# Performance work log

Hardware: AMD Instinct MI355X
Metric: run time of the kernel (lower is better)

The kernel has to match this reference:

```python
import jax, jax.numpy as jnp
import numpy as np
import math

N_HEADS = 8
NUM_LAYERS = 2
OUT_LEN = 96
MIN_FACTOR, MAX_FACTOR = 3, 10
MIN_KERNEL, MAX_KERNEL = 5, 51
LN_EPS = 1e-5


def layer_norm(x, g, b):
    mu = x.mean(-1, keepdims=True)
    var = x.var(-1, keepdims=True)  # biased, like nn.LayerNorm
    return (x - mu) / jnp.sqrt(var + LN_EPS) * g + b


def prob_sparse_attn(x, wq, bq, wk, bk, wv, bv, wo, bo):
    B, L, D = x.shape
    H, dk = N_HEADS, D // N_HEADS
    Q = (x @ wq + bq).reshape(B, L, H, dk).transpose(0, 2, 1, 3)  # [B,H,L,dk]
    K = (x @ wk + bk).reshape(B, L, H, dk).transpose(0, 2, 1, 3)
    V = (x @ wv + bv).reshape(B, L, H, dk).transpose(0, 2, 1, 3)
    # sparsity score per query: 0.5*||q|| + 0.3*entropy(softmax(q)) + 0.2*var(q)
    l2 = jnp.linalg.norm(Q, axis=-1)
    prob = jax.nn.softmax(Q, axis=-1)
    ent = -jnp.sum(prob * jnp.log(prob + 1e-9), axis=-1)
    var = Q.var(axis=-1, ddof=1)  # torch.var unbiased
    qs = 0.5 * l2 + 0.3 * ent + 0.2 * var  # [B,H,L]
    std = qs.std(axis=2, ddof=1)
    mean = qs.mean(axis=2)
    factor = jnp.clip(jnp.round(std / (mean + 1e-6) * MAX_FACTOR), MIN_FACTOR, MAX_FACTOR).astype(jnp.int32)  # [B,H]
    u = factor[:, 0]  # torch uses k_list[b][0]: head-0 factor per batch
    umax = min(MAX_FACTOR, L)
    _, top_idx = jax.lax.top_k(qs, umax)  # [B,H,umax]
    keep = jnp.arange(umax)[None, None, :] < u[:, None, None]  # [B,1->H,umax]
    Qs = jnp.take_along_axis(Q, top_idx[..., None], axis=2)  # [B,H,umax,dk]
    scores = jnp.einsum('bhud,bhld->bhul', Qs, K) / math.sqrt(dk)
    attn = jax.nn.softmax(scores, axis=-1)
    out = jnp.einsum('bhul,bhld->bhud', attn, V)  # [B,H,umax,dk]
    # scatter selected query outputs back; rows beyond u[b] are dropped (OOB index L)
    idx = jnp.where(keep, top_idx, L)
    full = jnp.zeros((B, H, L, dk), x.dtype)
    bI = jnp.arange(B)[:, None, None]
    hI = jnp.arange(H)[None, :, None]
    full = full.at[bI, hI, idx].set(out, mode='drop')
    y = full.transpose(0, 2, 1, 3).reshape(B, L, D)
    return y @ wo + bo


def adaptive_decomp(x):
    B, L, D = x.shape
    spec = jnp.abs(jnp.fft.rfft(x, axis=1)).mean(axis=(0, 2))
    peak = jnp.argmax(spec[1:]) + 1
    period = jnp.clip(L // peak, MIN_KERNEL, MAX_KERNEL)
    period = jnp.where(period % 2 == 0, period + 1, period)
    pad = period // 2
    # avg_pool1d(kernel=period, stride=1, padding=pad, count_include_pad=False) via cumsum
    t = jnp.arange(L)
    start = jnp.clip(t - pad, 0, L)
    end = jnp.clip(t + pad + 1, 0, L)
    cs = jnp.concatenate([jnp.zeros((B, 1, D), x.dtype), jnp.cumsum(x, axis=1)], axis=1)
    cnt = (end - start).astype(x.dtype)[None, :, None]
    trend = (cs[:, end] - cs[:, start]) / cnt
    return x - trend, trend


def _forward(x, w_embed, b_embed, wq, bq, wk, bk, wv, bv, wo, bo,
             w1, b1, w2, b2, g1, beta1, g2, beta2, w_out, b_out):
    h = x @ w_embed + b_embed
    for _ in range(NUM_LAYERS):  # share_params=True: same weights each layer
        a = prob_sparse_attn(h, wq, bq, wk, bk, wv, bv, wo, bo)
        h = layer_norm(h + a, g1, beta1)
        ffn = jax.nn.relu(h @ w1 + b1) @ w2 + b2
        h = layer_norm(h + ffn, g2, beta2)
    seasonal, trend = adaptive_decomp(h)
    combined = seasonal + trend
    out_seq = combined[:, -OUT_LEN:, :]
    pred = (out_seq @ w_out + b_out)[..., 0]  # [B, OUT_LEN]
    return pred


def setup_inputs() -> dict:
    key = jax.random.key(0)
    ks = jax.random.split(key, 16)
    B, L, Din, D, Dff = 16, 4096, 8, 512, 2048
    w = lambda k, shp: (jax.random.normal(k, shp, jnp.float32) * 0.02)
    return {
        'x': jax.random.normal(ks[0], (B, L, Din), jnp.float32),
        'w_embed': w(ks[1], (Din, D)), 'b_embed': jnp.zeros((D,), jnp.float32),
        'wq': w(ks[2], (D, D)), 'bq': jnp.zeros((D,), jnp.float32),
        'wk': w(ks[3], (D, D)), 'bk': jnp.zeros((D,), jnp.float32),
        'wv': w(ks[4], (D, D)), 'bv': jnp.zeros((D,), jnp.float32),
        'wo': w(ks[5], (D, D)), 'bo': jnp.zeros((D,), jnp.float32),
        'w1': w(ks[6], (D, Dff)), 'b1': jnp.zeros((Dff,), jnp.float32),
        'w2': w(ks[7], (Dff, D)), 'b2': jnp.zeros((D,), jnp.float32),
        'g1': jnp.ones((D,), jnp.float32), 'beta1': jnp.zeros((D,), jnp.float32),
        'g2': jnp.ones((D,), jnp.float32), 'beta2': jnp.zeros((D,), jnp.float32),
        'w_out': w(ks[8], (D, 1)), 'b_out': jnp.zeros((1,), jnp.float32),
    }


def reference(x, w_embed, b_embed, wq, bq, wk, bk, wv, bv, wo, bo,
              w1, b1, w2, b2, g1, beta1, g2, beta2, w_out, b_out):
    return _forward(x, w_embed, b_embed, wq, bq, wk, bk, wv, bv, wo, bo,
                    w1, b1, w2, b2, g1, beta1, g2, beta2, w_out, b_out)
```

## Files before the change

kernel.cpp:

```cpp
#include <hip/hip_runtime.h>
#include <math.h>

#define BB 16
#define LL 4096
#define DIN 8
#define DD 512
#define HH 8
#define DKK 64
#define DFF 2048
#define OUTLEN 96
#define TAIL0 (LL - OUTLEN)
#define NTAIL (BB * OUTLEN)
#define UMAX 10
#define CH 8192
#define QKVN 1536
#define NB 4
#define QM (NB * LL)
#define NSPLIT 32
#define LCHUNK (LL / NSPLIT)
#define PSTRIDE 68
#define MAXSLOT 128

typedef unsigned short ushort_t;
typedef unsigned int uint_t;
typedef short bf16x8 __attribute__((ext_vector_type(8)));
typedef float f32x4 __attribute__((ext_vector_type(4)));

#define GLD16(gp, lp) __builtin_amdgcn_global_load_lds((const __attribute__((address_space(1))) void*)(gp), (__attribute__((address_space(3))) void*)(lp), 16, 0, 0)

__device__ inline float wsum(float v){
#pragma unroll
  for (int o = 32; o > 0; o >>= 1) v += __shfl_xor(v, o);
  return v;
}
__device__ inline float wmax(float v){
#pragma unroll
  for (int o = 32; o > 0; o >>= 1) v = fmaxf(v, __shfl_xor(v, o));
  return v;
}
__device__ inline ushort_t f2bf_rtn(float f){
  uint_t u = __float_as_uint(f);
  uint_t r = u + 0x7FFF + ((u >> 16) & 1);
  return (ushort_t)(r >> 16);
}
__device__ inline float bf2f(ushort_t u){
  return __uint_as_float(((uint_t)u) << 16);
}
__device__ inline void split2(float x, ushort_t& hi, ushort_t& lo){
  uint_t u = __float_as_uint(x);
  hi = (ushort_t)(u >> 16);
  lo = f2bf_rtn(x - __uint_as_float(u & 0xFFFF0000u));
}
__device__ inline void xcd_map(int& bx, int& by){
  const int gx = gridDim.x;
  const int nwg = gx * gridDim.y;
  const int wg = (int)blockIdx.y * gx + (int)blockIdx.x;
  const int q = nwg >> 3, r = nwg & 7;
  const int xcd = wg & 7, idx = wg >> 3;
  const int swz = (xcd < r ? xcd * (q + 1) : r * (q + 1) + (xcd - r) * q) + idx;
  bx = swz % gx; by = swz / gx;
}

__global__ __launch_bounds__(256) void embed_kernel(const float* __restrict__ x,
    const float* __restrict__ we, const float* __restrict__ be,
    ushort_t* __restrict__ hh, ushort_t* __restrict__ hl){
  int row = blockIdx.x;
  __shared__ float xs[DIN];
  if (threadIdx.x < DIN) xs[threadIdx.x] = x[(size_t)row * DIN + threadIdx.x];
  __syncthreads();
  const int t = threadIdx.x;
  const int j0 = 2 * t;
  float a0 = be[j0], a1 = be[j0 + 1];
#pragma unroll
  for (int i = 0; i < DIN; ++i){
    a0 += xs[i] * we[i * DD + j0];
    a1 += xs[i] * we[i * DD + j0 + 1];
  }
  ushort_t h0, l0, h1, l1;
  split2(a0, h0, l0); split2(a1, h1, l1);
  ((uint_t*)(hh + (size_t)row * DD))[t] = (uint_t)h0 | ((uint_t)h1 << 16);
  ((uint_t*)(hl + (size_t)row * DD))[t] = (uint_t)l0 | ((uint_t)l1 << 16);
}

__global__ __launch_bounds__(256) void wsplit_t_kernel(const float* __restrict__ W,
    ushort_t* __restrict__ Th, ushort_t* __restrict__ Tl, int K, int N){
  int idx = blockIdx.x * 256 + threadIdx.x;
  if (idx >= N * K) return;
  int n = idx / K, k = idx - n * K;
  ushort_t hi, lo;
  split2(W[(size_t)k * N + n], hi, lo);
  Th[idx] = hi; Tl[idx] = lo;
}
__global__ __launch_bounds__(256) void wqkv_prep_kernel(const float* __restrict__ wq,
    const float* __restrict__ wk, const float* __restrict__ wv,
    ushort_t* __restrict__ Th, ushort_t* __restrict__ Tl){
  int idx = blockIdx.x * 256 + threadIdx.x;
  if (idx >= QKVN * DD) return;
  int n = idx >> 9, k = idx & (DD - 1);
  const float* src = (n < 512) ? wq : (n < 1024) ? wk : wv;
  ushort_t hi, lo;
  split2(src[(size_t)k * DD + (n & 511)], hi, lo);
  Th[idx] = hi; Tl[idx] = lo;
}
__global__ __launch_bounds__(256) void bqkv_prep_kernel(const float* __restrict__ bq,
    const float* __restrict__ bk, const float* __restrict__ bv, float* __restrict__ bo_){
  int n = blockIdx.x * 256 + threadIdx.x;
  if (n >= QKVN) return;
  bo_[n] = (n < 512) ? bq[n] : (n < 1024) ? bk[n - 512] : bv[n - 1024];
}

__global__ __launch_bounds__(256) void gemm_qkv(
    const ushort_t* __restrict__ Ah, const ushort_t* __restrict__ Al,
    const ushort_t* __restrict__ Bh, const ushort_t* __restrict__ Bl,
    const float* __restrict__ bias, float* __restrict__ Q,
    ushort_t* __restrict__ KV){
  __shared__ __align__(16) ushort_t AsH[128 * 32];
  __shared__ __align__(16) ushort_t AsL[128 * 32];
  __shared__ __align__(16) ushort_t BsH[128 * 32];
  __shared__ __align__(16) ushort_t BsL[128 * 32];
  int bx, by; xcd_map(bx, by);
  const int tid  = threadIdx.x;
  const int lane = tid & 63;
  const int wv   = tid >> 6;
  const int m0   = by * 128;
  const int n0   = bx * 128;
  const bool isQ = (n0 < 512);
  const int wm   = (wv & 1) * 64;
  const int wn   = (wv >> 1) * 64;

  const int rowA = tid >> 2;
  const int qe   = (tid & 3) * 8;
  const int lds0 = tid * 8;
  const int lds1 = (tid + 256) * 8;

  f32x4 acc[4][4];
#pragma unroll
  for (int i = 0; i < 4; ++i)
#pragma unroll
    for (int j = 0; j < 4; ++j) acc[i][j] = (f32x4){0.f, 0.f, 0.f, 0.f};

  const int arow = lane & 15;
  const int koff = (lane >> 4) * 8;
  const int K = DD;

  for (int k0 = 0; k0 < K; k0 += 32){
    const size_t ga0 = (size_t)(m0 + rowA) * K + k0 + qe;
    const size_t ga1 = (size_t)(m0 + rowA + 64) * K + k0 + qe;
    const size_t gb0 = (size_t)(n0 + rowA) * K + k0 + qe;
    const size_t gb1 = (size_t)(n0 + rowA + 64) * K + k0 + qe;
    GLD16(Ah + ga0, &AsH[lds0]);  GLD16(Ah + ga1, &AsH[lds1]);
    GLD16(Al + ga0, &AsL[lds0]);  GLD16(Al + ga1, &AsL[lds1]);
    GLD16(Bh + gb0, &BsH[lds0]);  GLD16(Bh + gb1, &BsH[lds1]);
    if (isQ){ GLD16(Bl + gb0, &BsL[lds0]);  GLD16(Bl + gb1, &BsL[lds1]); }
    __syncthreads();

    bf16x8 ah[4], al[4], bh[4], bl[4];
#pragma unroll
    for (int i = 0; i < 4; ++i){
      ah[i] = *(const bf16x8*)&AsH[(wm + i * 16 + arow) * 32 + koff];
      al[i] = *(const bf16x8*)&AsL[(wm + i * 16 + arow) * 32 + koff];
      bh[i] = *(const bf16x8*)&BsH[(wn + i * 16 + arow) * 32 + koff];
      if (isQ) bl[i] = *(const bf16x8*)&BsL[(wn + i * 16 + arow) * 32 + koff];
    }
#pragma unroll
    for (int i = 0; i < 4; ++i)
#pragma unroll
      for (int j = 0; j < 4; ++j){
        acc[i][j] = __builtin_amdgcn_mfma_f32_16x16x32_bf16(ah[i], bh[j], acc[i][j], 0, 0, 0);
        acc[i][j] = __builtin_amdgcn_mfma_f32_16x16x32_bf16(al[i], bh[j], acc[i][j], 0, 0, 0);
        if (isQ)
          acc[i][j] = __builtin_amdgcn_mfma_f32_16x16x32_bf16(ah[i], bl[j], acc[i][j], 0, 0, 0);
      }
    __syncthreads();
  }

  const int crow = (lane >> 4) * 4;
  const int ccol = lane & 15;
#pragma unroll
  for (int i = 0; i < 4; ++i){
    const int gr0 = m0 + wm + i * 16 + crow;
#pragma unroll
    for (int j = 0; j < 4; ++j){
      const int gc = n0 + wn + j * 16 + ccol;
      const float bvv = bias[gc];
#pragma unroll
      for (int r = 0; r < 4; ++r){
        float v = acc[i][j][r] + bvv;
        const int gr = gr0 + r;
        if (isQ) Q[(size_t)gr * 512 + gc] = v;
        else     KV[(size_t)gr * 1024 + (gc - 512)] = f2bf_rtn(v);
      }
    }
  }
}

__global__ __launch_bounds__(256) void gemm_ffn1(
    const ushort_t* __restrict__ Ah, const ushort_t* __restrict__ Al,
    const ushort_t* __restrict__ Bh, const float* __restrict__ bias,
    ushort_t* __restrict__ Chid){
  __shared__ __align__(16) ushort_t AsH[128 * 32];
  __shared__ __align__(16) ushort_t AsL[128 * 32];
  __shared__ __align__(16) ushort_t BsH[128 * 32];
  int bx, by; xcd_map(bx, by);
  const int tid  = threadIdx.x;
  const int lane = tid & 63;
  const int wv   = tid >> 6;
  const int m0   = by * 128;
  const int n0   = bx * 128;
  const int wm   = (wv & 1) * 64;
  const int wn   = (wv >> 1) * 64;
  const int rowA = tid >> 2;
  const int qe   = (tid & 3) * 8;
  const int lds0 = tid * 8;
  const int lds1 = (tid + 256) * 8;

  f32x4 acc[4][4];
#pragma unroll
  for (int i = 0; i < 4; ++i)
#pragma unroll
    for (int j = 0; j < 4; ++j) acc[i][j] = (f32x4){0.f, 0.f, 0.f, 0.f};

  const int arow = lane & 15;
  const int koff = (lane >> 4) * 8;
  const int K = DD;

  for (int k0 = 0; k0 < K; k0 += 32){
    const size_t ga0 = (size_t)(m0 + rowA) * K + k0 + qe;
    const size_t ga1 = (size_t)(m0 + rowA + 64) * K + k0 + qe;
    const size_t gb0 = (size_t)(n0 + rowA) * K + k0 + qe;
    const size_t gb1 = (size_t)(n0 + rowA + 64) * K + k0 + qe;
    GLD16(Ah + ga0, &AsH[lds0]);  GLD16(Ah + ga1, &AsH[lds1]);
    GLD16(Al + ga0, &AsL[lds0]);  GLD16(Al + ga1, &AsL[lds1]);
    GLD16(Bh + gb0, &BsH[lds0]);  GLD16(Bh + gb1, &BsH[lds1]);
    __syncthreads();

    bf16x8 ah[4], al[4], bh[4];
#pragma unroll
    for (int i = 0; i < 4; ++i){
      ah[i] = *(const bf16x8*)&AsH[(wm + i * 16 + arow) * 32 + koff];
      al[i] = *(const bf16x8*)&AsL[(wm + i * 16 + arow) * 32 + koff];
      bh[i] = *(const bf16x8*)&BsH[(wn + i * 16 + arow) * 32 + koff];
    }
#pragma unroll
    for (int i = 0; i < 4; ++i)
#pragma unroll
      for (int j = 0; j < 4; ++j){
        acc[i][j] = __builtin_amdgcn_mfma_f32_16x16x32_bf16(ah[i], bh[j], acc[i][j], 0, 0, 0);
        acc[i][j] = __builtin_amdgcn_mfma_f32_16x16x32_bf16(al[i], bh[j], acc[i][j], 0, 0, 0);
      }
    __syncthreads();
  }

  const int crow = (lane >> 4) * 4;
  const int ccol = lane & 15;
#pragma unroll
  for (int i = 0; i < 4; ++i){
    const int gr0 = m0 + wm + i * 16 + crow;
#pragma unroll
    for (int j = 0; j < 4; ++j){
      const int gc = n0 + wn + j * 16 + ccol;
      const float bvv = bias[gc];
#pragma unroll
      for (int r = 0; r < 4; ++r){
        float v = fmaxf(acc[i][j][r] + bvv, 0.f);
        Chid[(size_t)(gr0 + r) * DFF + gc] = f2bf_rtn(v);
      }
    }
  }
}

__global__ __launch_bounds__(256) void gemm_ffn2(
    const ushort_t* __restrict__ Ahid,
    const ushort_t* __restrict__ Bh, const ushort_t* __restrict__ Bl,
    float* __restrict__ pbuf, size_t pstr){
  __shared__ __align__(16) ushort_t AsH[128 * 32];
  __shared__ __align__(16) ushort_t BsH[128 * 32];
  __shared__ __align__(16) ushort_t BsL[128 * 32];
  int bx, by; xcd_map(bx, by);
  const int tid  = threadIdx.x;
  const int lane = tid & 63;
  const int wv   = tid >> 6;
  const int nblk = bx >> 1;
  const int kq   = bx & 1;
  const int m0   = by * 128;
  const int n0   = nblk * 128;
  const int wm   = (wv & 1) * 64;
  const int wn   = (wv >> 1) * 64;
  const int rowA = tid >> 2;
  const int qe   = (tid & 3) * 8;
  const int lds0 = tid * 8;
  const int lds1 = (tid + 256) * 8;

  f32x4 acc[4][4];
#pragma unroll
  for (int i = 0; i < 4; ++i)
#pragma unroll
    for (int j = 0; j < 4; ++j) acc[i][j] = (f32x4){0.f, 0.f, 0.f, 0.f};

  const int arow = lane & 15;
  const int koff = (lane >> 4) * 8;
  const int K = DFF;
  const int kper = K / 2;
  const int kbeg = kq * kper;

  for (int k0 = kbeg; k0 < kbeg + kper; k0 += 32){
    const size_t ga0 = (size_t)(m0 + rowA) * K + k0 + qe;
    const size_t ga1 = (size_t)(m0 + rowA + 64) * K + k0 + qe;
    const size_t gb0 = (size_t)(n0 + rowA) * K + k0 + qe;
    const size_t gb1 = (size_t)(n0 + rowA + 64) * K + k0 + qe;
    GLD16(Ahid + ga0, &AsH[lds0]);  GLD16(Ahid + ga1, &AsH[lds1]);
    GLD16(Bh + gb0, &BsH[lds0]);    GLD16(Bh + gb1, &BsH[lds1]);
    GLD16(Bl + gb0, &BsL[lds0]);    GLD16(Bl + gb1, &BsL[lds1]);
    __syncthreads();

    bf16x8 ah[4], bh[4], bl[4];
#pragma unroll
    for (int i = 0; i < 4; ++i){
      ah[i] = *(const bf16x8*)&AsH[(wm + i * 16 + arow) * 32 + koff];
      bh[i] = *(const bf16x8*)&BsH[(wn + i * 16 + arow) * 32 + koff];
      bl[i] = *(const bf16x8*)&BsL[(wn + i * 16 + arow) * 32 + koff];
    }
#pragma unroll
    for (int i = 0; i < 4; ++i)
#pragma unroll
      for (int j = 0; j < 4; ++j){
        acc[i][j] = __builtin_amdgcn_mfma_f32_16x16x32_bf16(ah[i], bh[j], acc[i][j], 0, 0, 0);
        acc[i][j] = __builtin_amdgcn_mfma_f32_16x16x32_bf16(ah[i], bl[j], acc[i][j], 0, 0, 0);
      }
    __syncthreads();
  }

  const int crow = (lane >> 4) * 4;
  const int ccol = lane & 15;
#pragma unroll
  for (int i = 0; i < 4; ++i){
    const int gr0 = m0 + wm + i * 16 + crow;
#pragma unroll
    for (int j = 0; j < 4; ++j){
      const int gc = n0 + wn + j * 16 + ccol;
#pragma unroll
      for (int r = 0; r < 4; ++r)
        pbuf[(size_t)kq * pstr + (size_t)(gr0 + r) * DD + gc] = acc[i][j][r];
    }
  }
}

__global__ __launch_bounds__(256) void qs_kernel(const float* __restrict__ qbuf, float* __restrict__ qsb){
  int tid = threadIdx.x;
  int lane = tid & 63;
  int wv = tid >> 6;
  int rid = blockIdx.x * 4 + wv;
  int bloc = rid >> 15;
  int hh = (rid >> 12) & 7;
  int l  = rid & (LL - 1);
  float qv = qbuf[((size_t)bloc * LL + l) * DD + hh * DKK + lane];
  float l2 = sqrtf(wsum(qv * qv));
  float mx = wmax(qv);
  float e  = expf(qv - mx);
  float se = wsum(e);
  float p  = e / se;
  float ent = -wsum(p * logf(p + 1e-9f));
  float mu  = wsum(qv) * (1.0f / 64.0f);
  float dv  = qv - mu;
  float var = wsum(dv * dv) * (1.0f / 63.0f);
  float val = 0.5f * l2 + 0.3f * ent + 0.2f * var;
  if (lane == 0) qsb[(size_t)(bloc * HH + hh) * LL + l] = val;
}

__global__ __launch_bounds__(256) void select_kernel(const float* __restrict__ qsb,
    int* __restrict__ topidx, int* __restrict__ ufac, int qtr){
  __shared__ float vals[LL];
  __shared__ float bv[256];
  __shared__ int   bi[256];
  __shared__ int   widx_s;
  __shared__ double r1[256], r2[256];
  const int bloc = blockIdx.y;
  const int b = qtr * NB + bloc;
  int tid = threadIdx.x;
  if (blockIdx.x == 8){
    const float* row = qsb + (size_t)bloc * HH * LL;
    double s = 0.0, s2 = 0.0;
    for (int l = tid; l < LL; l += 256){ double v = row[l]; s += v; s2 += v * v; }
    r1[tid] = s; r2[tid] = s2; __syncthreads();
    for (int st = 128; st; st >>= 1){
      if (tid < st){ r1[tid] += r1[tid+st]; r2[tid] += r2[tid+st]; }
      __syncthreads();
    }
    if (tid == 0){
      double mean = r1[0] / (double)LL;
      double var  = (r2[0] - (double)LL * mean * mean) / (double)(LL - 1);
      if (var < 0.0) var = 0.0;
      double f = rint(sqrt(var) / (mean + 1e-6) * 10.0);
      if (f < 3.0) f = 3.0;
      if (f > 10.0) f = 10.0;
      ufac[b] = (int)f;
    }
    return;
  }
  int hh = blockIdx.x;
  const float* row = qsb + ((size_t)bloc * HH + hh) * LL;
  for (int l = tid; l < LL; l += 256) vals[l] = row[l];
  __syncthreads();
  float lmax = -INFINITY; int lidx = 0;
  for (int l = tid; l < LL; l += 256){
    float v = vals[l];
    if (v > lmax){ lmax = v; lidx = l; }
  }
  for (int it = 0; it < UMAX; ++it){
    bv[tid] = lmax; bi[tid] = lidx;
    __syncthreads();
    for (int st = 128; st; st >>= 1){
      if (tid < st){
        if (bv[tid+st] > bv[tid] || (bv[tid+st] == bv[tid] && bi[tid+st] < bi[tid])){
          bv[tid] = bv[tid+st]; bi[tid] = bi[tid+st];
        }
      }
      __syncthreads();
    }
    if (tid == 0){ topidx[(b * HH + hh) * UMAX + it] = bi[0]; widx_s = bi[0]; }
    __syncthreads();
    const int w = widx_s;
    if ((w & 255) == tid){
      vals[w] = -INFINITY;
      lmax = -INFINITY; lidx = 0;
      for (int l = tid; l < LL; l += 256){
        float v = vals[l];
        if (v > lmax){ lmax = v; lidx = l; }
      }
    }
    __syncthreads();
  }
}

__global__ void initslot_kernel(int* __restrict__ slotmap, int* __restrict__ scount){
  int i = blockIdx.x * 256 + threadIdx.x;
  if (i < BB * LL) slotmap[i] = -1;
  if (i < BB) scount[i] = 0;
}
__global__ __launch_bounds__(128) void slotbuild_kernel(const int* __restrict__ topidx,
    const int* __restrict__ ufac, int* __restrict__ slotmap, int* __restrict__ scount, int qtr){
  int t = threadIdx.x;
  int b = qtr * NB + blockIdx.x;
  if (t >= HH * UMAX) return;
  int hh = t / UMAX, rank = t % UMAX;
  if (rank >= ufac[b]) return;
  int qpos = topidx[(b * HH + hh) * UMAX + rank];
  int* cell = &slotmap[b * LL + qpos];
  int old = atomicCAS(cell, -1, -2);
  if (old == -1){
    int s = atomicAdd(&scount[b], 1);
    atomicExch(cell, s);
  }
}

__global__ __launch_bounds__(256) void attn_p1_kernel(const float* __restrict__ qbuf,
    const ushort_t* __restrict__ kvbuf,
    const int* __restrict__ topidx, const int* __restrict__ ufac,
    float* __restrict__ part, int qtr, int lmin){
  const int bloc = blockIdx.z;
  const int b = qtr * NB + bloc;
  const int hh = blockIdx.y;
  const int u = ufac[b];
  const int tid = threadIdx.x, lane = tid & 63, wv = tid >> 6;
  const int base = blockIdx.x * LCHUNK + wv * 32;

  const ushort_t* Kp = kvbuf + (size_t)bloc * LL * 1024 + hh * DKK + lane;
  const ushort_t* Vp = Kp + 512;
  float kreg[32], vreg[32];
#pragma unroll
  for (int i = 0; i < 32; ++i){
    kreg[i] = bf2f(Kp[(size_t)(base + i) * 1024]);
    vreg[i] = bf2f(Vp[(size_t)(base + i) * 1024]);
  }

  __shared__ float wm4[4], ws4[4];
  __shared__ float pvs[4][DKK];

  for (int rank = 0; rank < u; ++rank){
    const int qpos = topidx[(b * HH + hh) * UMAX + rank];
    if (qpos < lmin) continue;
    const float qv = qbuf[((size_t)bloc * LL + qpos) * DD + hh * DKK + lane];

    float sc[32];
    float mloc = -INFINITY;
#pragma unroll
    for (int i = 0; i < 32; ++i){
      float s = wsum(qv * kreg[i]) * 0.125f;
      sc[i] = s;
      mloc = fmaxf(mloc, s);
    }
    if (lane == 0) wm4[wv] = mloc;
    __syncthreads();
    const float M4 = fmaxf(fmaxf(wm4[0], wm4[1]), fmaxf(wm4[2], wm4[3]));

    float ssum = 0.f;
#pragma unroll
    for (int i = 0; i < 32; ++i){ float e = expf(sc[i] - M4); sc[i] = e; ssum += e; }

    float pv = 0.f;
#pragma unroll
    for (int i = 0; i < 32; ++i) pv += sc[i] * vreg[i];

    pvs[wv][lane] = pv;
    if (lane == 0) ws4[wv] = ssum;
    __syncthreads();
    if (wv == 0){
      const int rowid = hh * UMAX + rank;
      float* rec = part + (size_t)((bloc * HH * UMAX + rowid) * NSPLIT + blockIdx.x) * PSTRIDE;
      rec[lane] = pvs[0][lane] + pvs[1][lane] + pvs[2][lane] + pvs[3][lane];
      if (lane == 0){ rec[64] = M4; rec[65] = ws4[0] + ws4[1] + ws4[2] + ws4[3]; }
    }
    __syncthreads();
  }
}

__global__ __launch_bounds__(256) void attn_p2_kernel(const float* __restrict__ part,
    const float* __restrict__ wo, const int* __restrict__ topidx, const int* __restrict__ ufac,
    const int* __restrict__ slotmap, float* __restrict__ adelta, int qtr, int lmin){
  const int bloc = blockIdx.y;
  const int b = qtr * NB + bloc;
  const int rowid = blockIdx.x;
  const int hh = rowid / UMAX, rank = rowid % UMAX;
  if (rank >= ufac[b]) return;
  const int qpos = topidx[(b * HH + hh) * UMAX + rank];
  if (qpos < lmin) return;
  const int slot = slotmap[b * LL + qpos];

  const int tid = threadIdx.x;
  const float* pbase = part + (size_t)(bloc * HH * UMAX + rowid) * NSPLIT * PSTRIDE;
  __shared__ float pm[NSPLIT], ps[NSPLIT];
  __shared__ float orow[DKK];
  if (tid < NSPLIT){
    pm[tid] = pbase[(size_t)tid * PSTRIDE + 64];
    ps[tid] = pbase[(size_t)tid * PSTRIDE + 65];
  }
  __syncthreads();
  float M = -INFINITY;
#pragma unroll
  for (int i = 0; i < NSPLIT; ++i) M = fmaxf(M, pm[i]);
  float S = 0.f;
#pragma unroll
  for (int i = 0; i < NSPLIT; ++i) S += ps[i] * expf(pm[i] - M);
  if (tid < DKK){
    float acc = 0.f;
#pragma unroll
    for (int i = 0; i < NSPLIT; ++i)
      acc += pbase[(size_t)i * PSTRIDE + tid] * expf(pm[i] - M);
    orow[tid] = acc / S;
  }
  __syncthreads();
  float* drow = adelta + ((size_t)b * MAXSLOT + slot) * DD;
  for (int j = tid; j < DD; j += 256){
    float a = 0.f;
#pragma unroll
    for (int dd = 0; dd < DKK; ++dd) a += orow[dd] * wo[(size_t)(hh * DKK + dd) * DD + j];
    atomicAdd(&drow[j], a);
  }
}

__global__ void zero_kernel(float* __restrict__ p, size_t n){
  size_t i = (size_t)blockIdx.x * 256 + threadIdx.x;
  size_t stride = (size_t)gridDim.x * 256;
  for (; i < n; i += stride) p[i] = 0.f;
}

template<bool TAIL>
__global__ __launch_bounds__(256) void ln1_kernel(
    const ushort_t* __restrict__ hh_, const ushort_t* __restrict__ hl_,
    const float* __restrict__ bo,
    const int* __restrict__ slotmap, const float* __restrict__ adelta,
    ushort_t* __restrict__ oh, ushort_t* __restrict__ ol,
    const float* __restrict__ g, const float* __restrict__ bb){
  __shared__ float red[256];
  int r = blockIdx.x, tid = threadIdx.x;
  int b, l;
  if (TAIL){ b = r / OUTLEN; l = TAIL0 + (r % OUTLEN); }
  else     { b = r >> 12;    l = r & (LL - 1); }
  const size_t gi = ((size_t)b * LL + l) * DD;
  const int j0 = 2 * tid;
  const uint_t hp = *(const uint_t*)(hh_ + gi + j0);
  const uint_t lp = *(const uint_t*)(hl_ + gi + j0);
  const float2 bo2 = *(const float2*)&bo[j0];
  float v0 = bf2f((ushort_t)(hp & 0xFFFF)) + bf2f((ushort_t)(lp & 0xFFFF)) + bo2.x;
  float v1 = bf2f((ushort_t)(hp >> 16))    + bf2f((ushort_t)(lp >> 16))    + bo2.y;
  int s = slotmap[b * LL + l];
  if (s >= 0){
    const float2 dr = *(const float2*)&adelta[((size_t)b * MAXSLOT + s) * DD + j0];
    v0 += dr.x; v1 += dr.y;
  }
  red[tid] = v0 + v1; __syncthreads();
  for (int st = 128; st; st >>= 1){ if (tid < st) red[tid] += red[tid+st]; __syncthreads(); }
  float mu = red[0] * (1.0f / DD); __syncthreads();
  float d0 = v0 - mu, d1 = v1 - mu;
  red[tid] = d0*d0 + d1*d1; __syncthreads();
  for (int st = 128; st; st >>= 1){ if (tid < st) red[tid] += red[tid+st]; __syncthreads(); }
  float rstd = rsqrtf(red[0] * (1.0f / DD) + 1e-5f);
  const float2 g2 = *(const float2*)&g[j0];
  const float2 bb2 = *(const float2*)&bb[j0];
  float o0 = d0 * rstd * g2.x + bb2.x;
  float o1 = d1 * rstd * g2.y + bb2.y;
  const size_t oo = TAIL ? (size_t)r * DD : gi;
  ushort_t h0, l0, h1, l1;
  split2(o0, h0, l0); split2(o1, h1, l1);
  *(uint_t*)(oh + oo + j0) = (uint_t)h0 | ((uint_t)h1 << 16);
  *(uint_t*)(ol + oo + j0) = (uint_t)l0 | ((uint_t)l1 << 16);
}

template<bool TAIL>
__global__ __launch_bounds__(256) void ln2_kernel(
    const ushort_t* __restrict__ ih, const ushort_t* __restrict__ il,
    const float* __restrict__ pbuf, size_t pstr, const float* __restrict__ b2,
    ushort_t* __restrict__ oh, ushort_t* __restrict__ ol, float* __restrict__ ofp,
    const float* __restrict__ g, const float* __restrict__ bb, size_t rowoff){
  __shared__ float red[256];
  int r = blockIdx.x, tid = threadIdx.x;
  const size_t gi = (rowoff + r) * DD;
  const size_t pi = (size_t)r * DD;
  const int j0 = 2 * tid;
  const uint_t hp = *(const uint_t*)(ih + gi + j0);
  const uint_t lp = *(const uint_t*)(il + gi + j0);
  const float2 p0 = *(const float2*)&pbuf[pi + j0];
  const float2 p1 = *(const float2*)&pbuf[pstr + pi + j0];
  const float2 b22 = *(const float2*)&b2[j0];
  float v0 = bf2f((ushort_t)(hp & 0xFFFF)) + bf2f((ushort_t)(lp & 0xFFFF)) + p0.x + p1.x + b22.x;
  float v1 = bf2f((ushort_t)(hp >> 16))    + bf2f((ushort_t)(lp >> 16))    + p0.y + p1.y + b22.y;
  red[tid] = v0 + v1; __syncthreads();
  for (int st = 128; st; st >>= 1){ if (tid < st) red[tid] += red[tid+st]; __syncthreads(); }
  float mu = red[0] * (1.0f / DD); __syncthreads();
  float d0 = v0 - mu, d1 = v1 - mu;
  red[tid] = d0*d0 + d1*d1; __syncthreads();
  for (int st = 128; st; st >>= 1){ if (tid < st) red[tid] += red[tid+st]; __syncthreads(); }
  float rstd = rsqrtf(red[0] * (1.0f / DD) + 1e-5f);
  const float2 g2 = *(const float2*)&g[j0];
  const float2 bb2 = *(const float2*)&bb[j0];
  float o0 = d0 * rstd * g2.x + bb2.x;
  float o1 = d1 * rstd * g2.y + bb2.y;
  if (TAIL){
    ofp[pi + j0] = o0; ofp[pi + j0 + 1] = o1;
  } else {
    ushort_t h0, l0, h1, l1;
    split2(o0, h0, l0); split2(o1, h1, l1);
    *(uint_t*)(oh + gi + j0) = (uint_t)h0 | ((uint_t)h1 << 16);
    *(uint_t*)(ol + gi + j0) = (uint_t)l0 | ((uint_t)l1 << 16);
  }
}

__global__ __launch_bounds__(64) void pred_kernel(const float* __restrict__ ht,
    const float* __restrict__ wout, const float* __restrict__ bout, float* __restrict__ out){
  int r = blockIdx.x, lane = threadIdx.x;
  float acc = 0.f;
  for (int dd = lane; dd < DD; dd += 64) acc += ht[(size_t)r * DD + dd] * wout[dd];
  acc = wsum(acc);
  if (lane == 0) out[r] = acc + bout[0];
}

extern "C" void kernel_launch(void* const* d_in, const int* in_sizes, int n_in,
                              void* d_out, int out_size, void* d_ws, size_t ws_size,
                              hipStream_t stream){
  const float* x    = (const float*)d_in[0];
  const float* wemb = (const float*)d_in[1];
  const float* bemb = (const float*)d_in[2];
  const float* wq   = (const float*)d_in[3];
  const float* bq   = (const float*)d_in[4];
  const float* wk   = (const float*)d_in[5];
  const float* bk   = (const float*)d_in[6];
  const float* wv   = (const float*)d_in[7];
  const float* bvv  = (const float*)d_in[8];
  const float* wo   = (const float*)d_in[9];
  const float* bo   = (const float*)d_in[10];
  const float* w1   = (const float*)d_in[11];
  const float* b1   = (const float*)d_in[12];
  const float* w2   = (const float*)d_in[13];
  const float* b2   = (const float*)d_in[14];
  const float* g1   = (const float*)d_in[15];
  const float* be1  = (const float*)d_in[16];
  const float* g2   = (const float*)d_in[17];
  const float* be2  = (const float*)d_in[18];
  const float* wout = (const float*)d_in[19];
  const float* bout = (const float*)d_in[20];
  float* out = (float*)d_out;
  char* wsb  = (char*)d_ws;

  const size_t MiB = 1024 * 1024;
  const size_t NE  = (size_t)BB * LL * DD;

  size_t o = 0;
  ushort_t* hh    = (ushort_t*)(wsb + o); o += NE * 2;
  ushort_t* hl    = (ushort_t*)(wsb + o); o += NE * 2;
  char*     arena = wsb + o;              o += 64 * MiB;
  float*    qbuf  = (float*)arena;
  ushort_t* kvbuf = (ushort_t*)(arena + 32 * MiB);
  ushort_t* hid   = (ushort_t*)arena;
  float*    pbuf  = (float*)(arena + 32 * MiB);
  ushort_t* hidt  = (ushort_t*)arena;
  float*    pbuft = (float*)(arena + 32 * MiB);
  ushort_t* asht  = (ushort_t*)(arena + 48 * MiB);
  ushort_t* aslt  = (ushort_t*)(arena + 50 * MiB);
  ushort_t* wtqkvh = (ushort_t*)(wsb + o); o += (size_t)QKVN * DD * 2;
  ushort_t* wtqkvl = (ushort_t*)(wsb + o); o += (size_t)QKVN * DD * 2;
  ushort_t* w1th   = (ushort_t*)(wsb + o); o += (size_t)DFF * DD * 2;
  ushort_t* w2th   = (ushort_t*)(wsb + o); o += (size_t)DD * DFF * 2;
  ushort_t* w2tl   = (ushort_t*)(wsb + o); o += (size_t)DD * DFF * 2;
  ushort_t* w1tl   = (ushort_t*)(wsb + o); o += (size_t)DFF * DD * 2;
  float*    bqkv   = (float*)(wsb + o);  o += QKVN * 4;
  float*    qsb    = (float*)(wsb + o);  o += (size_t)NB * HH * LL * 4;
  float*    part   = (float*)(wsb + o);  o += (size_t)NB * HH * UMAX * NSPLIT * PSTRIDE * 4;
  float*    adelta = (float*)(wsb + o);  o += (size_t)BB * MAXSLOT * DD * 4;
  float*    htail  = (float*)(wsb + o);  o += (size_t)NTAIL * DD * 4;
  int*      slotmap= (int*)(wsb + o);    o += (size_t)BB * LL * 4;
  int*      scount = (int*)(wsb + o);    o += BB * 4;
  int*      topidx = (int*)(wsb + o);    o += (size_t)BB * HH * UMAX * 4;
  int*      ufac   = (int*)(wsb + o);    o += 64;

  wqkv_prep_kernel<<<(QKVN*DD + 255)/256, 256, 0, stream>>>(wq, wk, wv, wtqkvh, wtqkvl);
  bqkv_prep_kernel<<<(QKVN + 255)/256, 256, 0, stream>>>(bq, bk, bvv, bqkv);
  wsplit_t_kernel<<<(DFF*DD + 255)/256, 256, 0, stream>>>(w1, w1th, w1tl, DD, DFF);
  wsplit_t_kernel<<<(DD*DFF + 255)/256, 256, 0, stream>>>(w2, w2th, w2tl, DFF, DD);

  embed_kernel<<<BB * LL, 256, 0, stream>>>(x, wemb, bemb, hh, hl);

  for (int layer = 0; layer < 2; ++layer){
    const bool tail = (layer == 1);
    const int lmin = tail ? TAIL0 : 0;

    initslot_kernel<<<(BB*LL + 255)/256, 256, 0, stream>>>(slotmap, scount);
    zero_kernel<<<1024, 256, 0, stream>>>(adelta, (size_t)BB * MAXSLOT * DD);

    for (int qtr = 0; qtr < BB / NB; ++qtr){
      const size_t hoff = (size_t)qtr * QM * DD;
      gemm_qkv<<<dim3(QKVN/128, QM/128), 256, 0, stream>>>(
          hh + hoff, hl + hoff, wtqkvh, wtqkvl, bqkv, qbuf, kvbuf);
      qs_kernel<<<(NB*HH*LL)/4, 256, 0, stream>>>(qbuf, qsb);
      select_kernel<<<dim3(9, NB), 256, 0, stream>>>(qsb, topidx, ufac, qtr);
      slotbuild_kernel<<<NB, 128, 0, stream>>>(topidx, ufac, slotmap, scount, qtr);
      attn_p1_kernel<<<dim3(NSPLIT, HH, NB), 256, 0, stream>>>(
          qbuf, kvbuf, topidx, ufac, part, qtr, lmin);
      attn_p2_kernel<<<dim3(HH*UMAX, NB), 256, 0, stream>>>(
          part, wo, topidx, ufac, slotmap, adelta, qtr, lmin);
    }

    if (!tail){
      ln1_kernel<false><<<BB*LL, 256, 0, stream>>>(hh, hl, bo, slotmap, adelta, hh, hl, g1, be1);
      for (int c = 0; c < (BB*LL)/CH; ++c){
        const size_t roff = (size_t)c * CH;
        gemm_ffn1<<<dim3(DFF/128, CH/128), 256, 0, stream>>>(
            hh + roff * DD, hl + roff * DD, w1th, b1, hid);
        gemm_ffn2<<<dim3(8, CH/128), 256, 0, stream>>>(hid, w2th, w2tl, pbuf, (size_t)CH * DD);
        ln2_kernel<false><<<CH, 256, 0, stream>>>(
            hh, hl, pbuf, (size_t)CH * DD, b2, hh, hl, nullptr, g2, be2, roff);
      }
    } else {
      ln1_kernel<true><<<NTAIL, 256, 0, stream>>>(hh, hl, bo, slotmap, adelta, asht, aslt, g1, be1);
      gemm_ffn1<<<dim3(DFF/128, NTAIL/128), 256, 0, stream>>>(asht, aslt, w1th, b1, hidt);
      gemm_ffn2<<<dim3(8, NTAIL/128), 256, 0, stream>>>(hidt, w2th, w2tl, pbuft, (size_t)NTAIL * DD);
      ln2_kernel<true><<<NTAIL, 256, 0, stream>>>(
          asht, aslt, pbuft, (size_t)NTAIL * DD, b2, nullptr, nullptr, htail, g2, be2, 0);
      pred_kernel<<<NTAIL, 64, 0, stream>>>(htail, wout, bout, out);
    }
  }
  (void)in_sizes; (void)n_in; (void)out_size; (void)ws_size;
}
```

Before: 2.549 ms.

## Tile weight transposes, batch embed rows, drop FFN2 split-K, use shuffle LayerNorm

Weight transpose-and-split kernels now stage a 32x32 tile through shared memory, so global reads and writes are both coalesced. The embed kernel handles 16 rows per block and loads the weights once into registers. FFN2 no longer splits K in two with partial buffers, which removes the extra partial write and read in ln2 but halves that GEMM's grid. The LayerNorm kernels switch from tree reductions in shared memory to wave shuffles computing sum and sum of squares in one pass, which risks a little precision loss through the E[x^2]-mu^2 variance.

```diff
diff --git a/kernel.cpp b/kernel.cpp
--- a/kernel.cpp
+++ b/kernel.cpp
@@ -20,6 +20,7 @@
 #define LCHUNK (LL / NSPLIT)
 #define PSTRIDE 68
 #define MAXSLOT 128
+#define EROWS 16
 
 typedef unsigned short ushort_t;
 typedef unsigned int uint_t;
@@ -31,11 +32,6 @@
 __device__ inline float wsum(float v){
 #pragma unroll
   for (int o = 32; o > 0; o >>= 1) v += __shfl_xor(v, o);
-  return v;
-}
-__device__ inline float wmax(float v){
-#pragma unroll
-  for (int o = 32; o > 0; o >>= 1) v = fmaxf(v, __shfl_xor(v, o));
   return v;
 }
 __device__ inline ushort_t f2bf_rtn(float f){
@@ -64,43 +60,70 @@
 __global__ __launch_bounds__(256) void embed_kernel(const float* __restrict__ x,
     const float* __restrict__ we, const float* __restrict__ be,
     ushort_t* __restrict__ hh, ushort_t* __restrict__ hl){
-  int row = blockIdx.x;
-  __shared__ float xs[DIN];
-  if (threadIdx.x < DIN) xs[threadIdx.x] = x[(size_t)row * DIN + threadIdx.x];
+  const int row0 = blockIdx.x * EROWS;
+  __shared__ float xs[EROWS][DIN];
+  const int t = threadIdx.x;
+  if (t < EROWS * DIN) xs[t >> 3][t & 7] = x[(size_t)row0 * DIN + t];
   __syncthreads();
-  const int t = threadIdx.x;
   const int j0 = 2 * t;
-  float a0 = be[j0], a1 = be[j0 + 1];
-#pragma unroll
-  for (int i = 0; i < DIN; ++i){
-    a0 += xs[i] * we[i * DD + j0];
-    a1 += xs[i] * we[i * DD + j0 + 1];
-  }
-  ushort_t h0, l0, h1, l1;
-  split2(a0, h0, l0); split2(a1, h1, l1);
-  ((uint_t*)(hh + (size_t)row * DD))[t] = (uint_t)h0 | ((uint_t)h1 << 16);
-  ((uint_t*)(hl + (size_t)row * DD))[t] = (uint_t)l0 | ((uint_t)l1 << 16);
+  float w0[DIN], w1r[DIN];
+#pragma unroll
+  for (int i = 0; i < DIN; ++i){ w0[i] = we[i * DD + j0]; w1r[i] = we[i * DD + j0 + 1]; }
+  const float b0 = be[j0], b1 = be[j0 + 1];
+#pragma unroll
+  for (int rr = 0; rr < EROWS; ++rr){
+    float a0 = b0, a1 = b1;
+#pragma unroll
+    for (int i = 0; i < DIN; ++i){ a0 += xs[rr][i] * w0[i]; a1 += xs[rr][i] * w1r[i]; }
+    ushort_t h0, l0, h1, l1;
+    split2(a0, h0, l0); split2(a1, h1, l1);
+    ((uint_t*)(hh + (size_t)(row0 + rr) * DD))[t] = (uint_t)h0 | ((uint_t)h1 << 16);
+    ((uint_t*)(hl + (size_t)(row0 + rr) * DD))[t] = (uint_t)l0 | ((uint_t)l1 << 16);
+  }
 }
 
 __global__ __launch_bounds__(256) void wsplit_t_kernel(const float* __restrict__ W,
     ushort_t* __restrict__ Th, ushort_t* __restrict__ Tl, int K, int N){
-  int idx = blockIdx.x * 256 + threadIdx.x;
-  if (idx >= N * K) return;
-  int n = idx / K, k = idx - n * K;
-  ushort_t hi, lo;
-  split2(W[(size_t)k * N + n], hi, lo);
-  Th[idx] = hi; Tl[idx] = lo;
+  __shared__ float tile[32][33];
+  const int n0 = blockIdx.x * 32;
+  const int k0 = blockIdx.y * 32;
+  const int tr = threadIdx.x >> 5;
+  const int tc = threadIdx.x & 31;
+#pragma unroll
+  for (int rr = 0; rr < 4; ++rr)
+    tile[tr + rr * 8][tc] = W[(size_t)(k0 + tr + rr * 8) * N + n0 + tc];
+  __syncthreads();
+#pragma unroll
+  for (int rr = 0; rr < 4; ++rr){
+    const int n = n0 + tr + rr * 8;
+    ushort_t hi, lo;
+    split2(tile[tc][tr + rr * 8], hi, lo);
+    Th[(size_t)n * K + k0 + tc] = hi;
+    Tl[(size_t)n * K + k0 + tc] = lo;
+  }
 }
 __global__ __launch_bounds__(256) void wqkv_prep_kernel(const float* __restrict__ wq,
     const float* __restrict__ wk, const float* __restrict__ wv,
     ushort_t* __restrict__ Th, ushort_t* __restrict__ Tl){
-  int idx = blockIdx.x * 256 + threadIdx.x;
-  if (idx >= QKVN * DD) return;
-  int n = idx >> 9, k = idx & (DD - 1);
-  const float* src = (n < 512) ? wq : (n < 1024) ? wk : wv;
-  ushort_t hi, lo;
-  split2(src[(size_t)k * DD + (n & 511)], hi, lo);
-  Th[idx] = hi; Tl[idx] = lo;
+  __shared__ float tile[32][33];
+  const int n0 = blockIdx.x * 32;
+  const int k0 = blockIdx.y * 32;
+  const float* src = (n0 < 512) ? wq : (n0 < 1024) ? wk : wv;
+  const int nb = n0 & 511;
+  const int tr = threadIdx.x >> 5;
+  const int tc = threadIdx.x & 31;
+#pragma unroll
+  for (int rr = 0; rr < 4; ++rr)
+    tile[tr + rr * 8][tc] = src[(size_t)(k0 + tr + rr * 8) * DD + nb + tc];
+  __syncthreads();
+#pragma unroll
+  for (int rr = 0; rr < 4; ++rr){
+    const int n = n0 + tr + rr * 8;
+    ushort_t hi, lo;
+    split2(tile[tc][tr + rr * 8], hi, lo);
+    Th[(size_t)n * DD + k0 + tc] = hi;
+    Tl[(size_t)n * DD + k0 + tc] = lo;
+  }
 }
 __global__ __launch_bounds__(256) void bqkv_prep_kernel(const float* __restrict__ bq,
     const float* __restrict__ bk, const float* __restrict__ bv, float* __restrict__ bo_){
@@ -272,7 +295,7 @@
 __global__ __launch_bounds__(256) void gemm_ffn2(
     const ushort_t* __restrict__ Ahid,
     const ushort_t* __restrict__ Bh, const ushort_t* __restrict__ Bl,
-    float* __restrict__ pbuf, size_t pstr){
+    float* __restrict__ fbuf){
   __shared__ __align__(16) ushort_t AsH[128 * 32];
   __shared__ __align__(16) ushort_t BsH[128 * 32];
   __shared__ __align__(16) ushort_t BsL[128 * 32];
@@ -280,10 +303,8 @@
   const int tid  = threadIdx.x;
   const int lane = tid & 63;
   const int wv   = tid >> 6;
-  const int nblk = bx >> 1;
-  const int kq   = bx & 1;
   const int m0   = by * 128;
-  const int n0   = nblk * 128;
+  const int n0   = bx * 128;
   const int wm   = (wv & 1) * 64;
   const int wn   = (wv >> 1) * 64;
   const int rowA = tid >> 2;
@@ -300,10 +321,8 @@
   const int arow = lane & 15;
   const int koff = (lane >> 4) * 8;
   const int K = DFF;
-  const int kper = K / 2;
-  const int kbeg = kq * kper;
-
-  for (int k0 = kbeg; k0 < kbeg + kper; k0 += 32){
+
+  for (int k0 = 0; k0 < K; k0 += 32){
     const size_t ga0 = (size_t)(m0 + rowA) * K + k0 + qe;
     const size_t ga1 = (size_t)(m0 + rowA + 64) * K + k0 + qe;
     const size_t gb0 = (size_t)(n0 + rowA) * K + k0 + qe;
@@ -340,7 +359,7 @@
       const int gc = n0 + wn + j * 16 + ccol;
 #pragma unroll
       for (int r = 0; r < 4; ++r)
-        pbuf[(size_t)kq * pstr + (size_t)(gr0 + r) * DD + gc] = acc[i][j][r];
+        fbuf[(size_t)(gr0 + r) * DD + gc] = acc[i][j][r];
     }
   }
 }
@@ -355,7 +374,9 @@
   int l  = rid & (LL - 1);
   float qv = qbuf[((size_t)bloc * LL + l) * DD + hh * DKK + lane];
   float l2 = sqrtf(wsum(qv * qv));
-  float mx = wmax(qv);
+  float mx = qv;
+#pragma unroll
+  for (int o = 32; o > 0; o >>= 1) mx = fmaxf(mx, __shfl_xor(mx, o));
   float e  = expf(qv - mx);
   float se = wsum(e);
   float p  = e / se;
@@ -571,8 +592,9 @@
     const int* __restrict__ slotmap, const float* __restrict__ adelta,
     ushort_t* __restrict__ oh, ushort_t* __restrict__ ol,
     const float* __restrict__ g, const float* __restrict__ bb){
-  __shared__ float red[256];
+  __shared__ float ss[4], qq[4];
   int r = blockIdx.x, tid = threadIdx.x;
+  const int lane = tid & 63, wv = tid >> 6;
   int b, l;
   if (TAIL){ b = r / OUTLEN; l = TAIL0 + (r % OUTLEN); }
   else     { b = r >> 12;    l = r & (LL - 1); }
@@ -588,17 +610,20 @@
     const float2 dr = *(const float2*)&adelta[((size_t)b * MAXSLOT + s) * DD + j0];
     v0 += dr.x; v1 += dr.y;
   }
-  red[tid] = v0 + v1; __syncthreads();
-  for (int st = 128; st; st >>= 1){ if (tid < st) red[tid] += red[tid+st]; __syncthreads(); }
-  float mu = red[0] * (1.0f / DD); __syncthreads();
-  float d0 = v0 - mu, d1 = v1 - mu;
-  red[tid] = d0*d0 + d1*d1; __syncthreads();
-  for (int st = 128; st; st >>= 1){ if (tid < st) red[tid] += red[tid+st]; __syncthreads(); }
-  float rstd = rsqrtf(red[0] * (1.0f / DD) + 1e-5f);
+  float sm = v0 + v1, qm = v0 * v0 + v1 * v1;
+#pragma unroll
+  for (int o2 = 32; o2 > 0; o2 >>= 1){ sm += __shfl_xor(sm, o2); qm += __shfl_xor(qm, o2); }
+  if (lane == 0){ ss[wv] = sm; qq[wv] = qm; }
+  __syncthreads();
+  const float S = ss[0] + ss[1] + ss[2] + ss[3];
+  const float Qv = qq[0] + qq[1] + qq[2] + qq[3];
+  const float mu = S * (1.0f / DD);
+  float var = Qv * (1.0f / DD) - mu * mu;
+  const float rstd = rsqrtf(var + 1e-5f);
   const float2 g2 = *(const float2*)&g[j0];
   const float2 bb2 = *(const float2*)&bb[j0];
-  float o0 = d0 * rstd * g2.x + bb2.x;
-  float o1 = d1 * rstd * g2.y + bb2.y;
+  float o0 = (v0 - mu) * rstd * g2.x + bb2.x;
+  float o1 = (v1 - mu) * rstd * g2.y + bb2.y;
   const size_t oo = TAIL ? (size_t)r * DD : gi;
   ushort_t h0, l0, h1, l1;
   split2(o0, h0, l0); split2(o1, h1, l1);
@@ -609,32 +634,35 @@
 template<bool TAIL>
 __global__ __launch_bounds__(256) void ln2_kernel(
     const ushort_t* __restrict__ ih, const ushort_t* __restrict__ il,
-    const float* __restrict__ pbuf, size_t pstr, const float* __restrict__ b2,
+    const float* __restrict__ fbuf, const float* __restrict__ b2,
     ushort_t* __restrict__ oh, ushort_t* __restrict__ ol, float* __restrict__ ofp,
     const float* __restrict__ g, const float* __restrict__ bb, size_t rowoff){
-  __shared__ float red[256];
+  __shared__ float ss[4], qq[4];
   int r = blockIdx.x, tid = threadIdx.x;
+  const int lane = tid & 63, wv = tid >> 6;
   const size_t gi = (rowoff + r) * DD;
   const size_t pi = (size_t)r * DD;
   const int j0 = 2 * tid;
   const uint_t hp = *(const uint_t*)(ih + gi + j0);
   const uint_t lp = *(const uint_t*)(il + gi + j0);
-  const float2 p0 = *(const float2*)&pbuf[pi + j0];
-  const float2 p1 = *(const float2*)&pbuf[pstr + pi + j0];
+  const float2 p0 = *(const float2*)&fbuf[pi + j0];
   const float2 b22 = *(const float2*)&b2[j0];
-  float v0 = bf2f((ushort_t)(hp & 0xFFFF)) + bf2f((ushort_t)(lp & 0xFFFF)) + p0.x + p1.x + b22.x;
-  float v1 = bf2f((ushort_t)(hp >> 16))    + bf2f((ushort_t)(lp >> 16))    + p0.y + p1.y + b22.y;
-  red[tid] = v0 + v1; __syncthreads();
-  for (int st = 128; st; st >>= 1){ if (tid < st) red[tid] += red[tid+st]; __syncthreads(); }
-  float mu = red[0] * (1.0f / DD); __syncthreads();
-  float d0 = v0 - mu, d1 = v1 - mu;
-  red[tid] = d0*d0 + d1*d1; __syncthreads();
-  for (int st = 128; st; st >>= 1){ if (tid < st) red[tid] += red[tid+st]; __syncthreads(); }
-  float rstd = rsqrtf(red[0] * (1.0f / DD) + 1e-5f);
+  float v0 = bf2f((ushort_t)(hp & 0xFFFF)) + bf2f((ushort_t)(lp & 0xFFFF)) + p0.x + b22.x;
+  float v1 = bf2f((ushort_t)(hp >> 16))    + bf2f((ushort_t)(lp >> 16))    + p0.y + b22.y;
+  float sm = v0 + v1, qm = v0 * v0 + v1 * v1;
+#pragma unroll
+  for (int o2 = 32; o2 > 0; o2 >>= 1){ sm += __shfl_xor(sm, o2); qm += __shfl_xor(qm, o2); }
+  if (lane == 0){ ss[wv] = sm; qq[wv] = qm; }
+  __syncthreads();
+  const float S = ss[0] + ss[1] + ss[2] + ss[3];
+  const float Qv = qq[0] + qq[1] + qq[2] + qq[3];
+  const float mu = S * (1.0f / DD);
+  float var = Qv * (1.0f / DD) - mu * mu;
+  const float rstd = rsqrtf(var + 1e-5f);
   const float2 g2 = *(const float2*)&g[j0];
   const float2 bb2 = *(const float2*)&bb[j0];
-  float o0 = d0 * rstd * g2.x + bb2.x;
-  float o1 = d1 * rstd * g2.y + bb2.y;
+  float o0 = (v0 - mu) * rstd * g2.x + bb2.x;
+  float o1 = (v1 - mu) * rstd * g2.y + bb2.y;
   if (TAIL){
     ofp[pi + j0] = o0; ofp[pi + j0 + 1] = o1;
   } else {
@@ -691,9 +719,9 @@
   float*    qbuf  = (float*)arena;
   ushort_t* kvbuf = (ushort_t*)(arena + 32 * MiB);
   ushort_t* hid   = (ushort_t*)arena;
-  float*    pbuf  = (float*)(arena + 32 * MiB);
+  float*    fbuf  = (float*)(arena + 32 * MiB);
   ushort_t* hidt  = (ushort_t*)arena;
-  float*    pbuft = (float*)(arena + 32 * MiB);
+  float*    fbuft = (float*)(arena + 32 * MiB);
   ushort_t* asht  = (ushort_t*)(arena + 48 * MiB);
   ushort_t* aslt  = (ushort_t*)(arena + 50 * MiB);
   ushort_t* wtqkvh = (ushort_t*)(wsb + o); o += (size_t)QKVN * DD * 2;
@@ -712,12 +740,12 @@
   int*      topidx = (int*)(wsb + o);    o += (size_t)BB * HH * UMAX * 4;
   int*      ufac   = (int*)(wsb + o);    o += 64;
 
-  wqkv_prep_kernel<<<(QKVN*DD + 255)/256, 256, 0, stream>>>(wq, wk, wv, wtqkvh, wtqkvl);
+  wqkv_prep_kernel<<<dim3(QKVN/32, DD/32), 256, 0, stream>>>(wq, wk, wv, wtqkvh, wtqkvl);
   bqkv_prep_kernel<<<(QKVN + 255)/256, 256, 0, stream>>>(bq, bk, bvv, bqkv);
-  wsplit_t_kernel<<<(DFF*DD + 255)/256, 256, 0, stream>>>(w1, w1th, w1tl, DD, DFF);
-  wsplit_t_kernel<<<(DD*DFF + 255)/256, 256, 0, stream>>>(w2, w2th, w2tl, DFF, DD);
-
-  embed_kernel<<<BB * LL, 256, 0, stream>>>(x, wemb, bemb, hh, hl);
+  wsplit_t_kernel<<<dim3(DFF/32, DD/32), 256, 0, stream>>>(w1, w1th, w1tl, DD, DFF);
+  wsplit_t_kernel<<<dim3(DD/32, DFF/32), 256, 0, stream>>>(w2, w2th, w2tl, DFF, DD);
+
+  embed_kernel<<<(BB * LL) / EROWS, 256, 0, stream>>>(x, wemb, bemb, hh, hl);
 
   for (int layer = 0; layer < 2; ++layer){
     const bool tail = (layer == 1);
@@ -745,16 +773,16 @@
         const size_t roff = (size_t)c * CH;
         gemm_ffn1<<<dim3(DFF/128, CH/128), 256, 0, stream>>>(
             hh + roff * DD, hl + roff * DD, w1th, b1, hid);
-        gemm_ffn2<<<dim3(8, CH/128), 256, 0, stream>>>(hid, w2th, w2tl, pbuf, (size_t)CH * DD);
+        gemm_ffn2<<<dim3(DD/128, CH/128), 256, 0, stream>>>(hid, w2th, w2tl, fbuf);
         ln2_kernel<false><<<CH, 256, 0, stream>>>(
-            hh, hl, pbuf, (size_t)CH * DD, b2, hh, hl, nullptr, g2, be2, roff);
+            hh, hl, fbuf, b2, hh, hl, nullptr, g2, be2, roff);
       }
     } else {
       ln1_kernel<true><<<NTAIL, 256, 0, stream>>>(hh, hl, bo, slotmap, adelta, asht, aslt, g1, be1);
       gemm_ffn1<<<dim3(DFF/128, NTAIL/128), 256, 0, stream>>>(asht, aslt, w1th, b1, hidt);
-      gemm_ffn2<<<dim3(8, NTAIL/128), 256, 0, stream>>>(hidt, w2th, w2tl, pbuft, (size_t)NTAIL * DD);
+      gemm_ffn2<<<dim3(DD/128, NTAIL/128), 256, 0, stream>>>(hidt, w2th, w2tl, fbuft);
       ln2_kernel<true><<<NTAIL, 256, 0, stream>>>(
-          asht, aslt, pbuft, (size_t)NTAIL * DD, b2, nullptr, nullptr, htail, g2, be2, 0);
+          asht, aslt, fbuft, b2, nullptr, nullptr, htail, g2, be2, 0);
       pred_kernel<<<NTAIL, 64, 0, stream>>>(htail, wout, bout, out);
     }
   }
```

Result: slower. 2.691 ms (+5.6%).
